# Performance work log

Measured on AMD Instinct MI355X. Metric: run time of the kernel, lower is better.

The kernel has to match this reference:

```python
import jax, jax.numpy as jnp
import numpy as np

B, N, D, H = 1, 4096, 512, 8
HD = D // H


def setup_inputs() -> dict:
    key = jax.random.key(0)
    ks = jax.random.split(key, 12)
    s = 0.02  # weight init scale for numerical stability
    query = jax.random.normal(ks[0], (B, N, D), jnp.float32)
    key_t = jax.random.normal(ks[1], (B, N, D), jnp.float32)
    value = jax.random.normal(ks[2], (B, N, D), jnp.float32)
    Wq = jax.random.normal(ks[3], (D, D), jnp.float32) * s
    bq = jax.random.normal(ks[4], (D,), jnp.float32) * s
    Wk = jax.random.normal(ks[5], (D, D), jnp.float32) * s
    bk = jax.random.normal(ks[6], (D,), jnp.float32) * s
    Wv = jax.random.normal(ks[7], (D, D), jnp.float32) * s
    bv = jax.random.normal(ks[8], (D,), jnp.float32) * s
    Wo = jax.random.normal(ks[9], (D, D), jnp.float32) * s
    bo = jax.random.normal(ks[10], (D,), jnp.float32) * s
    # build sgconv_mat exactly as __init__: shifted nonneg adjacency, max-normalized,
    # then symmetric degree normalization D^-1/2 A D^-1/2 (gwmha_layer_num=1)
    A = jax.random.uniform(ks[11], (N, N), jnp.float32)
    A = A + A.min()
    A = A / A.max()
    deg = A.sum(1)
    dinv = 1.0 / jnp.sqrt(deg)
    sgconv_mat = (dinv[:, None] * A * dinv[None, :])[None]  # [1,N,N]
    return {"query": query, "key": key_t, "value": value,
            "Wq": Wq, "bq": bq, "Wk": Wk, "bk": bk, "Wv": Wv, "bv": bv,
            "Wo": Wo, "bo": bo, "sgconv_mat": sgconv_mat}


def reference(query, key, value, Wq, bq, Wk, bk, Wv, bv, Wo, bo, sgconv_mat):
    b, n, d = query.shape
    q = (query @ Wq.T + bq).reshape(b, n, H, HD)
    k = (key @ Wk.T + bk).reshape(b, n, H, HD)
    v = (value @ Wv.T + bv).reshape(b, n, H, HD)
    energy = jnp.einsum('bqhd,bkhd->bhqk', q, k)
    attn = jax.nn.softmax(energy / jnp.sqrt(jnp.float32(d)), axis=3)
    out = jnp.einsum('bhqk,bkhd->bqhd', attn, v).reshape(b, n, d)
    out = sgconv_mat @ out          # [1,N,N] @ [B,N,D] -> [B,N,D]
    return out @ Wo.T + bo
```

## Files before the change

### kernel.cpp

```cpp
#include <hip/hip_runtime.h>
#include <hip/hip_bf16.h>
#include <math.h>

typedef __bf16 bf16_t;
typedef __bf16 bf16x8 __attribute__((ext_vector_type(8)));
typedef float floatx4 __attribute__((ext_vector_type(4)));

typedef __attribute__((address_space(1))) void gvoid_t;
typedef __attribute__((address_space(3))) void lvoid_t;

static __device__ __forceinline__ void gload_lds16(const bf16_t* g, const bf16_t* l) {
    __builtin_amdgcn_global_load_lds((gvoid_t*)(size_t)g,
                                     (lvoid_t*)(unsigned)(size_t)l,
                                     16, 0, 0);
}

static __device__ __forceinline__ unsigned pack_bf2(float lo, float hi) {
    bf16_t a = (bf16_t)lo, b = (bf16_t)hi;
    return (unsigned)__builtin_bit_cast(unsigned short, a)
         | ((unsigned)__builtin_bit_cast(unsigned short, b) << 16);
}

static __device__ inline void store_c(float* C, size_t i, float v) { C[i] = v; }
static __device__ inline void store_c(bf16_t* C, size_t i, float v) { C[i] = (bf16_t)v; }

static __device__ inline void cvt8(const float* src, bf16_t* dst, size_t idx) {
    float4 a = *(const float4*)(src + idx);
    float4 c = *(const float4*)(src + idx + 4);
    uint4 u;
    u.x = pack_bf2(a.x, a.y);
    u.y = pack_bf2(a.z, a.w);
    u.z = pack_bf2(c.x, c.y);
    u.w = pack_bf2(c.z, c.w);
    *(uint4*)(dst + idx) = u;
}

template <typename TC>
__device__ inline void gemm_body128(
    const bf16_t* __restrict__ A, int lda,
    const bf16_t* __restrict__ B, int ldb,
    const float* __restrict__ bias_col, const float* __restrict__ bias_row,
    float cscale,
    TC* __restrict__ C, int ldc, int K, int m0, int n0)
{
    __shared__ bf16_t As[128 * 32];
    __shared__ bf16_t Bs[128 * 32];

    const int tid = threadIdx.x;
    const int lane = tid & 63, wave = tid >> 6;
    const int wm = wave & 1, wn = wave >> 1;
    const int lo16 = lane & 15, quad = lane >> 4;

    const int r0 = tid >> 2;
    const int s0 = tid & 3;
    const int c0 = s0 ^ ((r0 >> 1) & 3);
    const bf16_t* ga0 = A + (size_t)(m0 + r0) * lda + c0 * 8;
    const bf16_t* ga1 = A + (size_t)(m0 + 64 + r0) * lda + c0 * 8;
    const bf16_t* gb0 = B + (size_t)(n0 + r0) * ldb + c0 * 8;
    const bf16_t* gb1 = B + (size_t)(n0 + 64 + r0) * ldb + c0 * 8;
    const bf16_t* la0 = As + wave * 512;
    const bf16_t* la1 = As + 2048 + wave * 512;
    const bf16_t* lb0 = Bs + wave * 512;
    const bf16_t* lb1 = Bs + 2048 + wave * 512;

    int aoff[4], boff[4];
#pragma unroll
    for (int t = 0; t < 4; ++t) {
        const int ra = wm * 64 + t * 16 + lo16;
        aoff[t] = ra * 32 + ((quad ^ ((ra >> 1) & 3)) << 3);
        const int rb = wn * 64 + t * 16 + lo16;
        boff[t] = rb * 32 + ((quad ^ ((rb >> 1) & 3)) << 3);
    }

    floatx4 acc[4][4] = {};

    for (int k0 = 0; k0 < K; k0 += 32) {
        __syncthreads();
        gload_lds16(ga0 + k0, la0);
        gload_lds16(ga1 + k0, la1);
        gload_lds16(gb0 + k0, lb0);
        gload_lds16(gb1 + k0, lb1);
        __syncthreads();

        bf16x8 af[4], bfv[4];
#pragma unroll
        for (int t = 0; t < 4; ++t) {
            af[t]  = *(const bf16x8*)(As + aoff[t]);
            bfv[t] = *(const bf16x8*)(Bs + boff[t]);
        }
#pragma unroll
        for (int mt = 0; mt < 4; ++mt)
#pragma unroll
            for (int nt = 0; nt < 4; ++nt)
                acc[mt][nt] = __builtin_amdgcn_mfma_f32_16x16x32_bf16(
                    af[mt], bfv[nt], acc[mt][nt], 0, 0, 0);
    }

#pragma unroll
    for (int nt = 0; nt < 4; ++nt) {
        const int gn = n0 + wn * 64 + nt * 16 + lo16;
        const float bc = bias_col ? bias_col[gn] : 0.f;
#pragma unroll
        for (int mt = 0; mt < 4; ++mt) {
#pragma unroll
            for (int r = 0; r < 4; ++r) {
                const int gm = m0 + wm * 64 + mt * 16 + quad * 4 + r;
                float v = acc[mt][nt][r] + bc;
                if (bias_row) v += bias_row[gm];
                store_c(C, (size_t)gm * ldc + gn, v * cscale);
            }
        }
    }
}

__global__ __launch_bounds__(256) void prep(
    const float* __restrict__ query, const float* __restrict__ key, const float* __restrict__ value,
    const float* __restrict__ Wq, const float* __restrict__ Wk,
    const float* __restrict__ Wv, const float* __restrict__ Wo,
    bf16_t* qB, bf16_t* kB, bf16_t* vB,
    bf16_t* wqB, bf16_t* wkB, bf16_t* wvB, bf16_t* woB)
{
    const int b = blockIdx.x;
    const float* src; bf16_t* dst; size_t base;
    if      (b < 256) { src = query; dst = qB;  base = (size_t)b * 8192; }
    else if (b < 512) { src = key;   dst = kB;  base = (size_t)(b - 256) * 8192; }
    else if (b < 768) { src = value; dst = vB;  base = (size_t)(b - 512) * 8192; }
    else if (b < 800) { src = Wq;    dst = wqB; base = (size_t)(b - 768) * 8192; }
    else if (b < 832) { src = Wk;    dst = wkB; base = (size_t)(b - 800) * 8192; }
    else if (b < 864) { src = Wv;    dst = wvB; base = (size_t)(b - 832) * 8192; }
    else              { src = Wo;    dst = woB; base = (size_t)(b - 864) * 8192; }
#pragma unroll
    for (int it = 0; it < 4; ++it)
        cvt8(src, dst, base + (size_t)it * 2048 + threadIdx.x * 8);
}

__global__ __launch_bounds__(256) void proj_qkv(
    const bf16_t* __restrict__ qB, const bf16_t* __restrict__ wqB, const float* __restrict__ bq,
    const bf16_t* __restrict__ kB, const bf16_t* __restrict__ wkB, const float* __restrict__ bk,
    const bf16_t* __restrict__ wvB, const bf16_t* __restrict__ vB, const float* __restrict__ bv,
    bf16_t* __restrict__ q, bf16_t* __restrict__ k, bf16_t* __restrict__ vt, float qscale,
    const float* __restrict__ sg, bf16_t* __restrict__ sgb)
{
    const int b = blockIdx.x;
    if (b >= 384) {
        const size_t base = (size_t)(b - 384) * 8192;
#pragma unroll
        for (int it = 0; it < 4; ++it)
            cvt8(sg, sgb, base + (size_t)it * 2048 + threadIdx.x * 8);
        return;
    }
    const int i = b & 127;
    if (b < 256) {
        const int m0 = (i & 31) * 128, n0 = (i >> 5) * 128;
        if (b < 128)
            gemm_body128<bf16_t>(qB, 512, wqB, 512, bq, nullptr, qscale, q, 512, 512, m0, n0);
        else
            gemm_body128<bf16_t>(kB, 512, wkB, 512, bk, nullptr, 1.f, k, 512, 512, m0, n0);
    } else {
        const int m0 = (i & 3) * 128, n0 = (i >> 2) * 128;
        gemm_body128<bf16_t>(wvB, 512, vB, 512, nullptr, bv, 1.f, vt, 4096, 512, m0, n0);
    }
}

__global__ __launch_bounds__(256) void sgconv_full(
    const bf16_t* __restrict__ sgb, const bf16_t* __restrict__ aot,
    bf16_t* __restrict__ o2)
{
    const int i = blockIdx.x;
    const int m0 = (i & 63) * 64;
    const int n0 = (i >> 6) * 64;

    __shared__ bf16_t As[64 * 64];
    __shared__ bf16_t Bs[64 * 64];

    const int tid = threadIdx.x;
    const int lane = tid & 63, wave = tid >> 6;
    const int wm = wave & 1, wn = wave >> 1;
    const int lo16 = lane & 15, quad = lane >> 4;

    const int r0 = tid >> 3, s0 = tid & 7;
    const int c0 = s0 ^ (r0 & 7);
    const bf16_t* gaA = sgb + (size_t)(m0 + r0) * 4096 + c0 * 8;
    const bf16_t* gaB = aot + (size_t)(n0 + r0) * 4096 + c0 * 8;
    const bf16_t* laA0 = As + wave * 512;
    const bf16_t* laA1 = As + 2048 + wave * 512;
    const bf16_t* laB0 = Bs + wave * 512;
    const bf16_t* laB1 = Bs + 2048 + wave * 512;

    int aoff[2][2], boff[2][2];
#pragma unroll
    for (int t = 0; t < 2; ++t)
#pragma unroll
        for (int kk = 0; kk < 2; ++kk) {
            const int ra = wm * 32 + t * 16 + lo16;
            aoff[t][kk] = ra * 64 + (((kk * 4 + quad) ^ (ra & 7)) << 3);
            const int rb = wn * 32 + t * 16 + lo16;
            boff[t][kk] = rb * 64 + (((kk * 4 + quad) ^ (rb & 7)) << 3);
        }

    floatx4 acc[2][2] = {};

    for (int k0 = 0; k0 < 4096; k0 += 64) {
        __syncthreads();
        gload_lds16(gaA + k0, laA0);
        gload_lds16(gaA + (size_t)32 * 4096 + k0, laA1);
        gload_lds16(gaB + k0, laB0);
        gload_lds16(gaB + (size_t)32 * 4096 + k0, laB1);
        __syncthreads();

        bf16x8 af[2][2], bfv[2][2];
#pragma unroll
        for (int t = 0; t < 2; ++t)
#pragma unroll
            for (int kk = 0; kk < 2; ++kk) {
                af[t][kk]  = *(const bf16x8*)(As + aoff[t][kk]);
                bfv[t][kk] = *(const bf16x8*)(Bs + boff[t][kk]);
            }
#pragma unroll
        for (int mt = 0; mt < 2; ++mt)
#pragma unroll
            for (int nt = 0; nt < 2; ++nt)
#pragma unroll
                for (int kk = 0; kk < 2; ++kk)
                    acc[mt][nt] = __builtin_amdgcn_mfma_f32_16x16x32_bf16(
                        af[mt][kk], bfv[nt][kk], acc[mt][nt], 0, 0, 0);
    }

#pragma unroll
    for (int nt = 0; nt < 2; ++nt) {
        const int gn = n0 + wn * 32 + nt * 16 + lo16;
#pragma unroll
        for (int mt = 0; mt < 2; ++mt)
#pragma unroll
            for (int r = 0; r < 4; ++r) {
                const int gm = m0 + wm * 32 + mt * 16 + quad * 4 + r;
                o2[(size_t)gm * 512 + gn] = (bf16_t)acc[mt][nt][r];
            }
    }
}

__global__ __launch_bounds__(256) void out_proj(
    const bf16_t* __restrict__ o2, const bf16_t* __restrict__ woB,
    const float* __restrict__ bo, float* __restrict__ out)
{
    const int i = blockIdx.x, x = i & 7, t = i >> 3;
    const int n0 = (t & 7) * 64;
    const int m0 = ((t >> 3) * 8 + x) * 64;

    __shared__ bf16_t As[64 * 68];
    __shared__ bf16_t Bs[64 * 68];

    const int tid = threadIdx.x;
    const int lane = tid & 63, wave = tid >> 6;
    const int wm = wave & 1, wn = wave >> 1;
    const int lo16 = lane & 15, quad = lane >> 4;
    const int sr = tid >> 2, sc = (tid & 3) * 8;

    floatx4 acc[2][2] = {};

    for (int k0 = 0; k0 < 512; k0 += 32) {
        bf16x8 a0 = *(const bf16x8*)(o2 + (size_t)(m0 + sr) * 512 + k0 + sc);
        bf16x8 b0 = *(const bf16x8*)(woB + (size_t)(n0 + sr) * 512 + k0 + sc);
        __syncthreads();
        *(bf16x8*)(&As[sr * 68 + sc]) = a0;
        *(bf16x8*)(&Bs[sr * 68 + sc]) = b0;
        __syncthreads();

        bf16x8 af[2], bfv[2];
#pragma unroll
        for (int mt = 0; mt < 2; ++mt)
            af[mt] = *(const bf16x8*)(&As[(wm * 32 + mt * 16 + lo16) * 68 + quad * 8]);
#pragma unroll
        for (int nt = 0; nt < 2; ++nt)
            bfv[nt] = *(const bf16x8*)(&Bs[(wn * 32 + nt * 16 + lo16) * 68 + quad * 8]);
#pragma unroll
        for (int mt = 0; mt < 2; ++mt)
#pragma unroll
            for (int nt = 0; nt < 2; ++nt)
                acc[mt][nt] = __builtin_amdgcn_mfma_f32_16x16x32_bf16(
                    af[mt], bfv[nt], acc[mt][nt], 0, 0, 0);
    }

#pragma unroll
    for (int nt = 0; nt < 2; ++nt) {
        const int gn = n0 + wn * 32 + nt * 16 + lo16;
        const float bc = bo[gn];
#pragma unroll
        for (int mt = 0; mt < 2; ++mt)
#pragma unroll
            for (int r = 0; r < 4; ++r) {
                const int gm = m0 + wm * 32 + mt * 16 + quad * 4 + r;
                out[(size_t)gm * 512 + gn] = acc[mt][nt][r] + bc;
            }
    }
}

__global__ __launch_bounds__(256, 4) void flash_attn(
    const bf16_t* __restrict__ q, const bf16_t* __restrict__ kk,
    const bf16_t* __restrict__ vt, float* __restrict__ op,
    float* __restrict__ lp)
{
    const int fid = blockIdx.x;

    const int N = 4096, D = 512;
    const int h   = fid & 7;
    const int qb  = (fid >> 3) & 31;
    const int qtr = fid >> 8;
    const int t0  = qtr * 1024;

    const int tid = threadIdx.x;
    const int w = tid >> 6, lane = tid & 63;
    const int lo16 = lane & 15, quad = lane >> 4;

    __shared__ bf16_t Ks[64 * 72];
    __shared__ bf16_t Vs[64 * 72];
    __shared__ bf16_t Ps[4][32 * 72];

    const bf16_t* qp = q + (size_t)(qb * 128 + w * 32 + lo16) * D + h * 64 + quad * 8;
    bf16x8 qf[2][2];
    qf[0][0] = *(const bf16x8*)qp;
    qf[0][1] = *(const bf16x8*)(qp + 32);
    qf[1][0] = *(const bf16x8*)(qp + 16 * D);
    qf[1][1] = *(const bf16x8*)(qp + 16 * D + 32);

    const int srow = tid >> 2, sc = (tid & 3) * 16;
    const bf16_t* ksrc = kk + (size_t)(t0 + srow) * D + h * 64 + sc;
    const bf16_t* vsrc = vt + (size_t)(h * 64 + srow) * N + t0 + sc;
    bf16_t* kdst = &Ks[srow * 72 + sc];
    bf16_t* vdst = &Vs[srow * 72 + sc];

    bf16x8 ones;
#pragma unroll
    for (int i = 0; i < 8; ++i) ones[i] = (bf16_t)1.0f;

    floatx4 o[4][2] = {};
    floatx4 lacc[2] = {};

    bf16x8 kr0 = *(const bf16x8*)ksrc;
    bf16x8 kr1 = *(const bf16x8*)(ksrc + 8);
    bf16x8 vr0 = *(const bf16x8*)vsrc;
    bf16x8 vr1 = *(const bf16x8*)(vsrc + 8);

    for (int it = 0; it < 16; ++it) {
        __syncthreads();
        *(bf16x8*)kdst = kr0;  *(bf16x8*)(kdst + 8) = kr1;
        *(bf16x8*)vdst = vr0;  *(bf16x8*)(vdst + 8) = vr1;
        __syncthreads();
        if (it < 15) {
            const bf16_t* kn = ksrc + (size_t)(it + 1) * 64 * D;
            const bf16_t* vn = vsrc + (it + 1) * 64;
            kr0 = *(const bf16x8*)kn;  kr1 = *(const bf16x8*)(kn + 8);
            vr0 = *(const bf16x8*)vn;  vr1 = *(const bf16x8*)(vn + 8);
        }

        floatx4 s[4][2];
#pragma unroll
        for (int tt = 0; tt < 4; ++tt) {
            bf16x8 kf0 = *(const bf16x8*)(&Ks[(tt * 16 + lo16) * 72 + quad * 8]);
            bf16x8 kf1 = *(const bf16x8*)(&Ks[(tt * 16 + lo16) * 72 + 32 + quad * 8]);
#pragma unroll
            for (int qt = 0; qt < 2; ++qt) {
                floatx4 a = {};
                a = __builtin_amdgcn_mfma_f32_16x16x32_bf16(kf0, qf[qt][0], a, 0, 0, 0);
                a = __builtin_amdgcn_mfma_f32_16x16x32_bf16(kf1, qf[qt][1], a, 0, 0, 0);
                s[tt][qt] = a;
            }
        }
#pragma unroll
        for (int tt = 0; tt < 4; ++tt)
#pragma unroll
            for (int qt = 0; qt < 2; ++qt) {
                float e0 = __builtin_amdgcn_exp2f(s[tt][qt][0]);
                float e1 = __builtin_amdgcn_exp2f(s[tt][qt][1]);
                float e2 = __builtin_amdgcn_exp2f(s[tt][qt][2]);
                float e3 = __builtin_amdgcn_exp2f(s[tt][qt][3]);
                uint2 pk;
                pk.x = pack_bf2(e0, e1);
                pk.y = pack_bf2(e2, e3);
                *(uint2*)(&Ps[w][(qt * 16 + lo16) * 72 + tt * 16 + quad * 4]) = pk;
            }
#pragma unroll
        for (int ks = 0; ks < 2; ++ks) {
            bf16x8 pf0 = *(const bf16x8*)(&Ps[w][lo16 * 72 + ks * 32 + quad * 8]);
            bf16x8 pf1 = *(const bf16x8*)(&Ps[w][(16 + lo16) * 72 + ks * 32 + quad * 8]);
            lacc[0] = __builtin_amdgcn_mfma_f32_16x16x32_bf16(ones, pf0, lacc[0], 0, 0, 0);
            lacc[1] = __builtin_amdgcn_mfma_f32_16x16x32_bf16(ones, pf1, lacc[1], 0, 0, 0);
#pragma unroll
            for (int t = 0; t < 4; ++t) {
                bf16x8 vf = *(const bf16x8*)(&Vs[(t * 16 + lo16) * 72 + ks * 32 + quad * 8]);
                o[t][0] = __builtin_amdgcn_mfma_f32_16x16x32_bf16(vf, pf0, o[t][0], 0, 0, 0);
                o[t][1] = __builtin_amdgcn_mfma_f32_16x16x32_bf16(vf, pf1, o[t][1], 0, 0, 0);
            }
        }
    }

    const int g = fid & 255;
    float* opw = op + ((size_t)qtr * 256 + g) * 8192;
#pragma unroll
    for (int t = 0; t < 4; ++t)
#pragma unroll
        for (int pt = 0; pt < 2; ++pt)
#pragma unroll
            for (int r = 0; r < 4; ++r)
                opw[(t * 16 + quad * 4 + r) * 128 + w * 32 + pt * 16 + lo16] = o[t][pt][r];

    if (quad == 0) {
        float* lpw = lp + ((size_t)qtr * 256 + g) * 128;
        lpw[w * 32 + lo16] = lacc[0][0];
        lpw[w * 32 + 16 + lo16] = lacc[1][0];
    }
}

__global__ __launch_bounds__(256) void attn_combine(
    const float* __restrict__ op, const float* __restrict__ lp, bf16_t* __restrict__ aot)
{
    const int bid = blockIdx.x;
    const int g = bid >> 2, qu = bid & 3;
    const int h = g & 7, qb = g >> 3;
    const int tid = threadIdx.x;
    __shared__ float ls[128];
    if (tid < 128) {
        float s = 0.f;
#pragma unroll
        for (int qtr = 0; qtr < 4; ++qtr)
            s += lp[((size_t)qtr * 256 + g) * 128 + tid];
        ls[tid] = 1.0f / s;
    }
    __syncthreads();
    const float* b0 = op + (size_t)g * 8192;
    const size_t QS = (size_t)256 * 8192;
#pragma unroll
    for (int i = 0; i < 8; ++i) {
        int idx = qu * 2048 + i * 256 + tid;
        float v = b0[idx] + b0[QS + idx] + b0[2 * QS + idx] + b0[3 * QS + idx];
        int dim = idx >> 7, qc = idx & 127;
        aot[(size_t)(h * 64 + dim) * 4096 + qb * 128 + qc] = (bf16_t)(v * ls[qc]);
    }
}

extern "C" void kernel_launch(void* const* d_in, const int* in_sizes, int n_in,
                              void* d_out, int out_size, void* d_ws, size_t ws_size,
                              hipStream_t stream)
{
    const int N = 4096, D = 512;
    const float* query = (const float*)d_in[0];
    const float* key_t = (const float*)d_in[1];
    const float* value = (const float*)d_in[2];
    const float* Wq = (const float*)d_in[3];
    const float* bq = (const float*)d_in[4];
    const float* Wk = (const float*)d_in[5];
    const float* bk = (const float*)d_in[6];
    const float* Wv = (const float*)d_in[7];
    const float* bv = (const float*)d_in[8];
    const float* Wo = (const float*)d_in[9];
    const float* bo = (const float*)d_in[10];
    const float* sg = (const float*)d_in[11];
    float* out = (float*)d_out;

    const size_t ND = (size_t)N * D;
    const size_t DD = (size_t)D * D;

    char* base = (char*)d_ws;
    bf16_t* q    = (bf16_t*)base;
    bf16_t* kk   = q   + ND;
    bf16_t* vt   = kk  + ND;
    bf16_t* aot  = vt  + ND;
    bf16_t* sgb  = aot + ND;
    char* regA   = (char*)(sgb + (size_t)N * N);
    bf16_t* qB   = (bf16_t*)regA;
    bf16_t* kB   = qB + ND;
    bf16_t* vB   = kB + ND;
    bf16_t* wqB  = vB + ND;
    bf16_t* wkB  = wqB + DD;
    bf16_t* wvB  = wkB + DD;
    float* op    = (float*)regA;
    char* tail   = regA + (size_t)4 * 256 * 8192 * 4;
    float*  lp   = (float*)tail;
    bf16_t* woB  = (bf16_t*)(lp + (size_t)4 * 256 * 128);
    bf16_t* o2   = woB + DD;

    const dim3 blk(256);

    prep<<<896, blk, 0, stream>>>(query, key_t, value, Wq, Wk, Wv, Wo,
                                  qB, kB, vB, wqB, wkB, wvB, woB);

    const float qscale = 1.44269504088896f / sqrtf((float)D);
    proj_qkv<<<2432, blk, 0, stream>>>(qB, wqB, bq, kB, wkB, bk,
                                       wvB, vB, bv, q, kk, vt, qscale, sg, sgb);

    flash_attn<<<1024, blk, 0, stream>>>(q, kk, vt, op, lp);
    attn_combine<<<1024, blk, 0, stream>>>(op, lp, aot);

    sgconv_full<<<512, blk, 0, stream>>>(sgb, aot, o2);
    out_proj<<<512, blk, 0, stream>>>(o2, woB, bo, out);

    (void)in_sizes; (void)n_in; (void)out_size; (void)ws_size;
}
```

Baseline: 256.7 us.

## Split sgconv GEMM K dimension in two and sum partials in out_proj

The N×N by N×D sgconv GEMM now runs as a split-K over two halves of K. It launches 1024 blocks instead of 512, which fills more compute units, and each half writes its own bf16 partial buffer. out_proj loads both partials and adds them elementwise before staging into LDS. This trades extra partial-buffer traffic and an extra bf16 rounding step for shorter per-block K loops and higher occupancy. The workspace must have room for a second ND buffer after o2.

After: 246.6 us. 3.9% less time.

```diff
diff --git a/kernel.cpp b/kernel.cpp
--- a/kernel.cpp
+++ b/kernel.cpp
@@ -23,6 +23,13 @@
 
 static __device__ inline void store_c(float* C, size_t i, float v) { C[i] = v; }
 static __device__ inline void store_c(bf16_t* C, size_t i, float v) { C[i] = (bf16_t)v; }
+
+static __device__ __forceinline__ bf16x8 add8(bf16x8 a, bf16x8 b) {
+    bf16x8 r;
+#pragma unroll
+    for (int i = 0; i < 8; ++i) r[i] = (bf16_t)((float)a[i] + (float)b[i]);
+    return r;
+}
 
 static __device__ inline void cvt8(const float* src, bf16_t* dst, size_t idx) {
     float4 a = *(const float4*)(src + idx);
@@ -162,13 +169,16 @@
     }
 }
 
-__global__ __launch_bounds__(256) void sgconv_full(
+__global__ __launch_bounds__(256) void sgconv_half(
     const bf16_t* __restrict__ sgb, const bf16_t* __restrict__ aot,
-    bf16_t* __restrict__ o2)
-{
-    const int i = blockIdx.x;
+    bf16_t* __restrict__ o2p)
+{
+    const int bid = blockIdx.x;
+    const int i = bid & 511;
+    const int kb = bid >> 9;
     const int m0 = (i & 63) * 64;
     const int n0 = (i >> 6) * 64;
+    const int kbase = kb * 2048;
 
     __shared__ bf16_t As[64 * 64];
     __shared__ bf16_t Bs[64 * 64];
@@ -180,8 +190,8 @@
 
     const int r0 = tid >> 3, s0 = tid & 7;
     const int c0 = s0 ^ (r0 & 7);
-    const bf16_t* gaA = sgb + (size_t)(m0 + r0) * 4096 + c0 * 8;
-    const bf16_t* gaB = aot + (size_t)(n0 + r0) * 4096 + c0 * 8;
+    const bf16_t* gaA = sgb + (size_t)(m0 + r0) * 4096 + kbase + c0 * 8;
+    const bf16_t* gaB = aot + (size_t)(n0 + r0) * 4096 + kbase + c0 * 8;
     const bf16_t* laA0 = As + wave * 512;
     const bf16_t* laA1 = As + 2048 + wave * 512;
     const bf16_t* laB0 = Bs + wave * 512;
@@ -200,7 +210,7 @@
 
     floatx4 acc[2][2] = {};
 
-    for (int k0 = 0; k0 < 4096; k0 += 64) {
+    for (int k0 = 0; k0 < 2048; k0 += 64) {
         __syncthreads();
         gload_lds16(gaA + k0, laA0);
         gload_lds16(gaA + (size_t)32 * 4096 + k0, laA1);
@@ -226,6 +236,7 @@
                         af[mt][kk], bfv[nt][kk], acc[mt][nt], 0, 0, 0);
     }
 
+    bf16_t* dst = o2p + (size_t)kb * (4096 * 512);
 #pragma unroll
     for (int nt = 0; nt < 2; ++nt) {
         const int gn = n0 + wn * 32 + nt * 16 + lo16;
@@ -234,13 +245,14 @@
 #pragma unroll
             for (int r = 0; r < 4; ++r) {
                 const int gm = m0 + wm * 32 + mt * 16 + quad * 4 + r;
-                o2[(size_t)gm * 512 + gn] = (bf16_t)acc[mt][nt][r];
+                dst[(size_t)gm * 512 + gn] = (bf16_t)acc[mt][nt][r];
             }
     }
 }
 
 __global__ __launch_bounds__(256) void out_proj(
-    const bf16_t* __restrict__ o2, const bf16_t* __restrict__ woB,
+    const bf16_t* __restrict__ o2a, const bf16_t* __restrict__ o2b,
+    const bf16_t* __restrict__ woB,
     const float* __restrict__ bo, float* __restrict__ out)
 {
     const int i = blockIdx.x, x = i & 7, t = i >> 3;
@@ -259,7 +271,8 @@
     floatx4 acc[2][2] = {};
 
     for (int k0 = 0; k0 < 512; k0 += 32) {
-        bf16x8 a0 = *(const bf16x8*)(o2 + (size_t)(m0 + sr) * 512 + k0 + sc);
+        const size_t aidx = (size_t)(m0 + sr) * 512 + k0 + sc;
+        bf16x8 a0 = add8(*(const bf16x8*)(o2a + aidx), *(const bf16x8*)(o2b + aidx));
         bf16x8 b0 = *(const bf16x8*)(woB + (size_t)(n0 + sr) * 512 + k0 + sc);
         __syncthreads();
         *(bf16x8*)(&As[sr * 68 + sc]) = a0;
@@ -478,6 +491,7 @@
     float*  lp   = (float*)tail;
     bf16_t* woB  = (bf16_t*)(lp + (size_t)4 * 256 * 128);
     bf16_t* o2   = woB + DD;
+    bf16_t* o2b  = o2 + ND;
 
     const dim3 blk(256);
 
@@ -491,8 +505,8 @@
     flash_attn<<<1024, blk, 0, stream>>>(q, kk, vt, op, lp);
     attn_combine<<<1024, blk, 0, stream>>>(op, lp, aot);
 
-    sgconv_full<<<512, blk, 0, stream>>>(sgb, aot, o2);
-    out_proj<<<512, blk, 0, stream>>>(o2, woB, bo, out);
+    sgconv_half<<<1024, blk, 0, stream>>>(sgb, aot, o2);
+    out_proj<<<512, blk, 0, stream>>>(o2, o2b, woB, bo, out);
 
     (void)in_sizes; (void)n_in; (void)out_size; (void)ws_size;
 }
```
